# Performance work log

Hardware: AMD Instinct MI355X
Metric: run time of the kernel (lower is better)

## Reference

```python
import jax, jax.numpy as jnp
import numpy as np

E = 8          # num_experts
R = 16         # lora rank
TOP_K = 2
SCALING = 32.0 / 16.0   # lora_alpha / r
D_IN = 4096
D_OUT = 4096


def setup_inputs() -> dict:
    key = jax.random.key(0)
    ks = jax.random.split(key, 6)
    x = jax.random.normal(ks[0], (4, 2048, D_IN), jnp.float32)
    Wb = jax.random.normal(ks[1], (D_OUT, D_IN), jnp.float32) * 0.02
    bias = jax.random.normal(ks[2], (D_OUT,), jnp.float32) * 0.02
    Wr = jax.random.normal(ks[3], (E, D_IN), jnp.float32) * 0.01  # router (normal init, std=0.01)
    A = jax.random.normal(ks[4], (E, R, D_IN), jnp.float32) * (1.0 / np.sqrt(D_IN))  # kaiming-ish
    Bm = jax.random.normal(ks[5], (E, D_OUT, R), jnp.float32) * 0.01  # nonzero for nontrivial baseline
    return {"x": x, "Wb": Wb, "bias": bias, "Wr": Wr, "A": A, "Bm": Bm}


def reference(x, Wb, bias, Wr, A, Bm):
    # x: [B, S, D_IN]
    xf = x.reshape(-1, x.shape[-1])                       # [T, D_IN]
    T = xf.shape[0]

    # Router: softmax -> top-k -> renormalize selected probs
    logits = xf @ Wr.T                                    # [T, E]
    probs = jax.nn.softmax(logits, axis=-1)
    topk_p, topk_i = jax.lax.top_k(probs, TOP_K)          # [T, K]
    topk_p = topk_p / jnp.sum(topk_p, axis=-1, keepdims=True)

    # Dense per-token expert weights via scatter-add (equivalent to masked dispatch/combine)
    w = jnp.zeros((T, E), xf.dtype).at[jnp.arange(T)[:, None], topk_i].add(topk_p)  # [T, E]

    # LoRA: x @ A_e^T @ B_e^T, weighted combine (dropout = identity, p=0)
    h = jnp.einsum('ti,eri->ter', xf, A)                  # [T, E, R] (small: rank-16)
    lora = jnp.einsum('ter,te,eor->to', h, w, Bm) * SCALING  # [T, D_OUT]

    base = xf @ Wb.T + bias                               # [T, D_OUT]
    out = (base + lora).reshape(*x.shape[:-1], D_OUT)
    return out
```

## Files before the change

kernel.cpp:

```cpp
#include <hip/hip_runtime.h>
#include <cmath>

typedef unsigned short ushort_t;
typedef __attribute__((ext_vector_type(8))) short short8;
typedef __attribute__((ext_vector_type(4))) float f32x4;

#define D_IN   4096
#define D_OUT  4096
#define T_TOK  8192
#define E_EXP  8
#define R_RANK 16
#define KCAT   4224
#define SCALE_LORA 2.0f

__device__ __forceinline__ ushort_t f2bf(float f) {
    unsigned int u = __float_as_uint(f);
    u += 0x7fffu + ((u >> 16) & 1u);
    return (ushort_t)(u >> 16);
}

__global__ __launch_bounds__(256) void build_weights(
    const float* __restrict__ Wb, const float* __restrict__ Bm,
    const float* __restrict__ A, ushort_t* __restrict__ Wcat,
    ushort_t* __restrict__ Abf) {
    int b = blockIdx.x;
    int tid = threadIdx.x;
    if (b < D_OUT) {
        const float4* src = (const float4*)(Wb + (size_t)b * D_IN);
        ushort_t* drow = Wcat + (size_t)b * KCAT;
        for (int c4 = tid; c4 < D_IN / 4; c4 += 256) {
            float4 v = src[c4];
            ushort4 o;
            o.x = f2bf(v.x); o.y = f2bf(v.y); o.z = f2bf(v.z); o.w = f2bf(v.w);
            ((ushort4*)drow)[c4] = o;
        }
        if (tid < E_EXP * R_RANK) {
            int e = tid >> 4, r = tid & 15;
            drow[D_IN + tid] = f2bf(Bm[((size_t)e * D_OUT + b) * R_RANK + r]);
        }
    } else {
        int er = b - D_OUT;
        const float4* src = (const float4*)(A + (size_t)er * D_IN);
        ushort_t* drow = Abf + (size_t)er * D_IN;
        for (int c4 = tid; c4 < D_IN / 4; c4 += 256) {
            float4 v = src[c4];
            ushort4 o;
            o.x = f2bf(v.x); o.y = f2bf(v.y); o.z = f2bf(v.z); o.w = f2bf(v.w);
            ((ushort4*)drow)[c4] = o;
        }
    }
}

__global__ __launch_bounds__(256) void router_convert(
    const float* __restrict__ x, const float* __restrict__ Wr,
    ushort_t* __restrict__ xcat, int2* __restrict__ eids,
    float2* __restrict__ wts) {
    __shared__ float sWr[E_EXP * D_IN];
    int tid = threadIdx.x;
    int lane = tid & 63;
    int wave = tid >> 6;
    int tbase = blockIdx.x * 16 + wave * 4;

    {
        const float4* wsrc = (const float4*)Wr;
        float4* wdst = (float4*)sWr;
#pragma unroll
        for (int q = 0; q < 32; q++)
            wdst[tid + q * 256] = wsrc[tid + q * 256];
    }
    __syncthreads();

    float acc[4][E_EXP];
#pragma unroll
    for (int tk = 0; tk < 4; tk++)
#pragma unroll
        for (int e = 0; e < E_EXP; e++) acc[tk][e] = 0.f;

    for (int c4 = lane; c4 < D_IN / 4; c4 += 64) {
        float4 wv[E_EXP];
#pragma unroll
        for (int e = 0; e < E_EXP; e++)
            wv[e] = ((const float4*)(sWr + (size_t)e * D_IN))[c4];
#pragma unroll
        for (int tk = 0; tk < 4; tk++) {
            int t = tbase + tk;
            float4 v = ((const float4*)(x + (size_t)t * D_IN))[c4];
            ushort4 o;
            o.x = f2bf(v.x); o.y = f2bf(v.y); o.z = f2bf(v.z); o.w = f2bf(v.w);
            ((ushort4*)(xcat + (size_t)t * KCAT))[c4] = o;
#pragma unroll
            for (int e = 0; e < E_EXP; e++)
                acc[tk][e] +=
                    v.x * wv[e].x + v.y * wv[e].y + v.z * wv[e].z + v.w * wv[e].w;
        }
    }

#pragma unroll
    for (int tk = 0; tk < 4; tk++)
#pragma unroll
        for (int e = 0; e < E_EXP; e++) {
#pragma unroll
            for (int off = 32; off > 0; off >>= 1)
                acc[tk][e] += __shfl_xor(acc[tk][e], off, 64);
        }
    if (lane == 0) {
#pragma unroll
        for (int tk = 0; tk < 4; tk++) {
            int t = tbase + tk;
            int e0 = 0; float l0 = acc[tk][0];
#pragma unroll
            for (int e = 1; e < E_EXP; e++)
                if (acc[tk][e] > l0) { l0 = acc[tk][e]; e0 = e; }
            int e1 = -1; float l1 = -3.4e38f;
#pragma unroll
            for (int e = 0; e < E_EXP; e++)
                if (e != e0 && acc[tk][e] > l1) { l1 = acc[tk][e]; e1 = e; }
            float w0 = 1.f / (1.f + expf(l1 - l0));
            eids[t] = make_int2(e0, e1);
            wts[t] = make_float2(w0, 1.f - w0);
        }
    }
}

__global__ __launch_bounds__(256) void h_gemm_v(
    const ushort_t* __restrict__ Abf, const int2* __restrict__ eids,
    const float2* __restrict__ wts, ushort_t* __restrict__ xcat) {
    __shared__ __align__(16) ushort_t lA[3][32 * 64];
    __shared__ __align__(16) ushort_t lB[3][128 * 64];
    int tid = threadIdx.x;
    int lane = tid & 63, wave = tid >> 6;
    int rowBase = blockIdx.x * 32;
    const ushort_t* gA = xcat + (size_t)rowBase * KCAT;

    const int srow = tid >> 3;
    const int scol = (((tid & 7) ^ (srow & 7)) << 3);

#define HSTAGE(BUF, KT)                                                        \
    {                                                                          \
        __builtin_amdgcn_global_load_lds(                                      \
            (const __attribute__((address_space(1))) unsigned int*)(           \
                gA + (size_t)srow * KCAT + (KT) + scol),                       \
            (__attribute__((address_space(3))) unsigned int*)(                 \
                &lA[BUF][0] + wave * 512), 16, 0, 0);                          \
        _Pragma("unroll")                                                      \
        for (int q = 0; q < 4; q++) {                                          \
            __builtin_amdgcn_global_load_lds(                                  \
                (const __attribute__((address_space(1))) unsigned int*)(       \
                    Abf + (size_t)(srow + 32 * q) * D_IN + (KT) + scol),       \
                (__attribute__((address_space(3))) unsigned int*)(             \
                    &lB[BUF][0] + q * 2048 + wave * 512), 16, 0, 0);           \
        }                                                                      \
    }

    f32x4 acc[2][2];
#pragma unroll
    for (int i = 0; i < 2; i++)
#pragma unroll
        for (int j = 0; j < 2; j++)
            acc[i][j] = (f32x4){0.f, 0.f, 0.f, 0.f};

    int n0 = wave * 32;
    int row16 = lane & 15;
    int cSwz[2];
#pragma unroll
    for (int kc = 0; kc < 2; kc++)
        cSwz[kc] = (kc * 64 + (lane >> 4) * 16) ^ ((row16 & 7) << 4);

    HSTAGE(0, 0)
    HSTAGE(1, 64)
    asm volatile("s_waitcnt vmcnt(5)" ::: "memory");
    __builtin_amdgcn_s_barrier();

    for (int t = 0; t < 64; ++t) {
        int cur = t % 3;
        int tn = (t + 2 < 64) ? (t + 2) : 63;
        HSTAGE((t + 2) % 3, tn * 64)
        asm volatile("s_waitcnt vmcnt(10)" ::: "memory");
        __builtin_amdgcn_s_barrier();

        short8 af[2][2], bfr[2][2];
#pragma unroll
        for (int i = 0; i < 2; i++)
#pragma unroll
            for (int kc = 0; kc < 2; kc++)
                af[i][kc] = *(const short8*)((const char*)&lA[cur][0] +
                    (i * 16 + row16) * 128 + cSwz[kc]);
#pragma unroll
        for (int j = 0; j < 2; j++)
#pragma unroll
            for (int kc = 0; kc < 2; kc++)
                bfr[j][kc] = *(const short8*)((const char*)&lB[cur][0] +
                    (n0 + j * 16 + row16) * 128 + cSwz[kc]);

        __builtin_amdgcn_s_setprio(1);
#pragma unroll
        for (int i = 0; i < 2; i++)
#pragma unroll
            for (int j = 0; j < 2; j++) {
                acc[i][j] = __builtin_amdgcn_mfma_f32_16x16x32_bf16(
                    af[i][0], bfr[j][0], acc[i][j], 0, 0, 0);
                acc[i][j] = __builtin_amdgcn_mfma_f32_16x16x32_bf16(
                    af[i][1], bfr[j][1], acc[i][j], 0, 0, 0);
            }
        __builtin_amdgcn_s_setprio(0);
        __builtin_amdgcn_s_barrier();
    }

#pragma unroll
    for (int i = 0; i < 2; i++) {
        int rbase = rowBase + i * 16 + (lane >> 4) * 4;
#pragma unroll
        for (int reg = 0; reg < 4; reg++) {
            int t = rbase + reg;
            int2 e = eids[t];
            float2 w = wts[t];
#pragma unroll
            for (int j = 0; j < 2; j++) {
                int c = n0 + j * 16 + (lane & 15);
                int ce = c >> 4;
                float coef = (ce == e.x) ? (SCALE_LORA * w.x)
                           : ((ce == e.y) ? (SCALE_LORA * w.y) : 0.f);
                xcat[(size_t)t * KCAT + D_IN + c] = f2bf(coef * acc[i][j][reg]);
            }
        }
    }
#undef HSTAGE
}

#define NKT 66
#define NIT 33

__global__ __launch_bounds__(512, 2) void gemm_bt_main(
    const ushort_t* __restrict__ Am, const ushort_t* __restrict__ Bmat,
    float* __restrict__ C, const float* __restrict__ bias) {
    __shared__ __align__(16) ushort_t lds[2][2][2][128][64];
    const int lda = KCAT, ldb = KCAT, ldc = D_OUT;
    int tid = threadIdx.x;
    int lane = tid & 63, wave = tid >> 6;
    int wm = wave >> 2, wn = wave & 3;

    int id = ((blockIdx.x & 7) << 6) | (blockIdx.x >> 3);
    int band = id >> 6, wi = id & 63;
    int mt = ((band >> 1) << 3) | (wi & 7);
    int nt = ((band & 1) << 3) | (wi >> 3);
    const int rowBase = mt * 256, colBase = nt * 256;

    const ushort_t* gA = Am + (size_t)rowBase * lda;
    const ushort_t* gB = Bmat + (size_t)colBase * ldb;

    const int srow = tid >> 3;
    const int scol = (((tid & 7) ^ (srow & 7)) << 3);

#define STAGE(MAT, SRC, LD, BUF, KT)                                           \
    {                                                                          \
        _Pragma("unroll")                                                      \
        for (int h = 0; h < 2; h++) {                                          \
            _Pragma("unroll")                                                  \
            for (int q = 0; q < 2; q++) {                                      \
                __builtin_amdgcn_global_load_lds(                              \
                    (const __attribute__((address_space(1))) unsigned int*)(   \
                        (SRC) + (size_t)(h * 128 + q * 64 + srow) * (LD) +     \
                        (KT) + scol),                                          \
                    (__attribute__((address_space(3))) unsigned int*)(         \
                        &lds[BUF][MAT][h][0][0] + q * 4096 + wave * 512),      \
                    16, 0, 0);                                                 \
            }                                                                  \
        }                                                                      \
    }

    int cSwz[2];
#pragma unroll
    for (int kc = 0; kc < 2; kc++)
        cSwz[kc] = (kc * 64 + (lane >> 4) * 16) ^ ((lane & 7) << 4);
    const int rOff = (lane & 15) * 128;
    const int bRow = (wn & 1) * 64 * 128;

    const char* baseA = (const char*)&lds[0][0][wm][0][0];
    const char* baseB = (const char*)&lds[0][1][wn >> 1][0][0];

    f32x4 acc[8][4];
#pragma unroll
    for (int i = 0; i < 8; i++)
#pragma unroll
        for (int j = 0; j < 4; j++) acc[i][j] = (f32x4){0.f, 0.f, 0.f, 0.f};

    short8 aF[4][2], bF[2][2];

#define READ_A(BUF, S)                                                         \
    _Pragma("unroll")                                                          \
    for (int m4 = 0; m4 < 4; m4++) {                                           \
        _Pragma("unroll")                                                      \
        for (int kc = 0; kc < 2; kc++)                                         \
            aF[m4][kc] = *(const short8*)(baseA + (BUF) * 65536 +              \
                ((S) * 4 + m4) * 2048 + rOff + cSwz[kc]);                      \
    }

#define READ_B(BUF, U)                                                         \
    _Pragma("unroll")                                                          \
    for (int n2 = 0; n2 < 2; n2++) {                                           \
        _Pragma("unroll")                                                      \
        for (int kc = 0; kc < 2; kc++)                                         \
            bF[n2][kc] = *(const short8*)(baseB + (BUF) * 65536 + bRow +       \
                ((U) * 2 + n2) * 2048 + rOff + cSwz[kc]);                      \
    }

#define MFMA16(S, U)                                                           \
    __builtin_amdgcn_s_setprio(1);                                             \
    _Pragma("unroll")                                                          \
    for (int m4 = 0; m4 < 4; m4++) {                                           \
        _Pragma("unroll")                                                      \
        for (int n2 = 0; n2 < 2; n2++) {                                       \
            _Pragma("unroll")                                                  \
            for (int kc = 0; kc < 2; kc++)                                     \
                acc[(S) * 4 + m4][(U) * 2 + n2] =                              \
                    __builtin_amdgcn_mfma_f32_16x16x32_bf16(                   \
                        aF[m4][kc], bF[n2][kc],                                \
                        acc[(S) * 4 + m4][(U) * 2 + n2], 0, 0, 0);             \
        }                                                                      \
    }                                                                          \
    __builtin_amdgcn_s_setprio(0);

#define MIDBAR()                                                               \
    __builtin_amdgcn_s_barrier();                                              \
    asm volatile("s_waitcnt lgkmcnt(0)" ::: "memory");

#define ENDBAR() __builtin_amdgcn_s_barrier();

    STAGE(0, gA, lda, 0, 0)
    STAGE(1, gB, ldb, 0, 0)
    STAGE(0, gA, lda, 1, 64)
    asm volatile("s_waitcnt vmcnt(4)" ::: "memory");
    __builtin_amdgcn_s_barrier();

    for (int it = 0; it < NIT; ++it) {
        int ktB1 = (2 * it + 1) * 64;
        int t2 = 2 * it + 2; if (t2 > NKT - 1) t2 = NKT - 1;
        int t3 = 2 * it + 3; if (t3 > NKT - 1) t3 = NKT - 1;
        int kt2 = t2 * 64, kt3 = t3 * 64;

        READ_A(0, 0) READ_B(0, 0)
        STAGE(1, gB, ldb, 1, ktB1)
        MIDBAR() MFMA16(0, 0) ENDBAR()

        READ_B(0, 1)
        MIDBAR() MFMA16(0, 1) ENDBAR()

        READ_A(0, 1)
        MIDBAR() MFMA16(1, 1) ENDBAR()

        READ_B(0, 0)
        STAGE(0, gA, lda, 0, kt2)
        MIDBAR() MFMA16(1, 0)
        asm volatile("s_waitcnt vmcnt(4)" ::: "memory");
        ENDBAR()

        READ_A(1, 0) READ_B(1, 0)
        STAGE(1, gB, ldb, 0, kt2)
        MIDBAR() MFMA16(0, 0) ENDBAR()

        READ_B(1, 1)
        MIDBAR() MFMA16(0, 1) ENDBAR()

        READ_A(1, 1)
        MIDBAR() MFMA16(1, 1) ENDBAR()

        READ_B(1, 0)
        STAGE(0, gA, lda, 1, kt3)
        MIDBAR() MFMA16(1, 0)
        asm volatile("s_waitcnt vmcnt(4)" ::: "memory");
        ENDBAR()
    }

    int r0 = rowBase + wm * 128 + (lane >> 4) * 4;
    int c0 = colBase + wn * 64 + (lane & 15);
#pragma unroll
    for (int mf = 0; mf < 8; mf++) {
#pragma unroll
        for (int nf = 0; nf < 4; nf++) {
            int cc = c0 + nf * 16;
            float badd = bias[cc];
#pragma unroll
            for (int reg = 0; reg < 4; reg++)
                C[(size_t)(r0 + mf * 16 + reg) * ldc + cc] = acc[mf][nf][reg] + badd;
        }
    }
}

extern "C" void kernel_launch(void* const* d_in, const int* in_sizes, int n_in,
                              void* d_out, int out_size, void* d_ws, size_t ws_size,
                              hipStream_t stream) {
    const float* x    = (const float*)d_in[0];
    const float* Wb   = (const float*)d_in[1];
    const float* bias = (const float*)d_in[2];
    const float* Wr   = (const float*)d_in[3];
    const float* A    = (const float*)d_in[4];
    const float* Bm   = (const float*)d_in[5];
    float* out = (float*)d_out;

    char* p = (char*)d_ws;
    ushort_t* xcat = (ushort_t*)p; p += (size_t)T_TOK * KCAT * 2;
    ushort_t* Wcat = (ushort_t*)p; p += (size_t)D_OUT * KCAT * 2;
    ushort_t* Abf  = (ushort_t*)p; p += (size_t)(E_EXP * R_RANK) * D_IN * 2;
    int2*     eids = (int2*)p;     p += (size_t)T_TOK * sizeof(int2);
    float2*   wts  = (float2*)p;   p += (size_t)T_TOK * sizeof(float2);

    build_weights<<<D_OUT + E_EXP * R_RANK, 256, 0, stream>>>(Wb, Bm, A, Wcat, Abf);
    router_convert<<<T_TOK / 16, 256, 0, stream>>>(x, Wr, xcat, eids, wts);
    h_gemm_v<<<T_TOK / 32, 256, 0, stream>>>(Abf, eids, wts, xcat);
    gemm_bt_main<<<(T_TOK / 256) * (D_OUT / 256), 512, 0, stream>>>(xcat, Wcat, out, bias);
}
```

Measured before the change: 559.8 us.

## Switch main GEMM to 32x32x16 MFMA and drop LDS staging in router

The main bf16 GEMM moves from 16x16x32 MFMA tiles to 32x32x16 tiles. This halves the instruction count and reduces LDS fragment reads per FLOP, and the fragment read schedule and epilogue store mapping are reworked to fit. Separately, the router kernel no longer copies the 128KB router weight matrix into shared memory. It reads it directly from global/L2 and processes 2 tokens per wave with twice as many blocks, which raises occupancy but re-reads Wr from cache more often.

```diff
diff --git a/kernel.cpp b/kernel.cpp
--- a/kernel.cpp
+++ b/kernel.cpp
@@ -4,6 +4,7 @@
 typedef unsigned short ushort_t;
 typedef __attribute__((ext_vector_type(8))) short short8;
 typedef __attribute__((ext_vector_type(4))) float f32x4;
+typedef __attribute__((ext_vector_type(16))) float f32x16;
 
 #define D_IN   4096
 #define D_OUT  4096
@@ -55,24 +56,14 @@
     const float* __restrict__ x, const float* __restrict__ Wr,
     ushort_t* __restrict__ xcat, int2* __restrict__ eids,
     float2* __restrict__ wts) {
-    __shared__ float sWr[E_EXP * D_IN];
     int tid = threadIdx.x;
     int lane = tid & 63;
     int wave = tid >> 6;
-    int tbase = blockIdx.x * 16 + wave * 4;
-
-    {
-        const float4* wsrc = (const float4*)Wr;
-        float4* wdst = (float4*)sWr;
-#pragma unroll
-        for (int q = 0; q < 32; q++)
-            wdst[tid + q * 256] = wsrc[tid + q * 256];
-    }
-    __syncthreads();
-
-    float acc[4][E_EXP];
-#pragma unroll
-    for (int tk = 0; tk < 4; tk++)
+    int tbase = blockIdx.x * 8 + wave * 2;
+
+    float acc[2][E_EXP];
+#pragma unroll
+    for (int tk = 0; tk < 2; tk++)
 #pragma unroll
         for (int e = 0; e < E_EXP; e++) acc[tk][e] = 0.f;
 
@@ -80,9 +71,9 @@
         float4 wv[E_EXP];
 #pragma unroll
         for (int e = 0; e < E_EXP; e++)
-            wv[e] = ((const float4*)(sWr + (size_t)e * D_IN))[c4];
-#pragma unroll
-        for (int tk = 0; tk < 4; tk++) {
+            wv[e] = ((const float4*)(Wr + (size_t)e * D_IN))[c4];
+#pragma unroll
+        for (int tk = 0; tk < 2; tk++) {
             int t = tbase + tk;
             float4 v = ((const float4*)(x + (size_t)t * D_IN))[c4];
             ushort4 o;
@@ -96,7 +87,7 @@
     }
 
 #pragma unroll
-    for (int tk = 0; tk < 4; tk++)
+    for (int tk = 0; tk < 2; tk++)
 #pragma unroll
         for (int e = 0; e < E_EXP; e++) {
 #pragma unroll
@@ -105,7 +96,7 @@
         }
     if (lane == 0) {
 #pragma unroll
-        for (int tk = 0; tk < 4; tk++) {
+        for (int tk = 0; tk < 2; tk++) {
             int t = tbase + tk;
             int e0 = 0; float l0 = acc[tk][0];
 #pragma unroll
@@ -268,54 +259,56 @@
         }                                                                      \
     }
 
-    int cSwz[2];
-#pragma unroll
-    for (int kc = 0; kc < 2; kc++)
-        cSwz[kc] = (kc * 64 + (lane >> 4) * 16) ^ ((lane & 7) << 4);
-    const int rOff = (lane & 15) * 128;
+    int kOff[4];
+#pragma unroll
+    for (int ks = 0; ks < 4; ks++)
+        kOff[ks] = (ks * 32 + ((lane >> 5) << 4)) ^ ((lane & 7) << 4);
+    const int rOff = (lane & 31) * 128;
     const int bRow = (wn & 1) * 64 * 128;
 
     const char* baseA = (const char*)&lds[0][0][wm][0][0];
-    const char* baseB = (const char*)&lds[0][1][wn >> 1][0][0];
-
-    f32x4 acc[8][4];
-#pragma unroll
-    for (int i = 0; i < 8; i++)
-#pragma unroll
-        for (int j = 0; j < 4; j++) acc[i][j] = (f32x4){0.f, 0.f, 0.f, 0.f};
-
-    short8 aF[4][2], bF[2][2];
-
-#define READ_A(BUF, S)                                                         \
+    const char* baseB = (const char*)&lds[0][1][wn >> 1][0][0] + bRow;
+
+    f32x16 acc[4][2];
+#pragma unroll
+    for (int i = 0; i < 4; i++)
+#pragma unroll
+        for (int j = 0; j < 2; j++)
+#pragma unroll
+            for (int r = 0; r < 16; r++) acc[i][j][r] = 0.f;
+
+    short8 A1[2][2], A2[2][2], bF[2][2];
+
+#define READ_AX(REG, BUF, MP, KP)                                              \
     _Pragma("unroll")                                                          \
-    for (int m4 = 0; m4 < 4; m4++) {                                           \
+    for (int m2 = 0; m2 < 2; m2++) {                                           \
         _Pragma("unroll")                                                      \
-        for (int kc = 0; kc < 2; kc++)                                         \
-            aF[m4][kc] = *(const short8*)(baseA + (BUF) * 65536 +              \
-                ((S) * 4 + m4) * 2048 + rOff + cSwz[kc]);                      \
-    }
-
-#define READ_B(BUF, U)                                                         \
+        for (int k2 = 0; k2 < 2; k2++)                                         \
+            REG[m2][k2] = *(const short8*)(baseA + (BUF) * 65536 +             \
+                ((MP) * 2 + m2) * 4096 + rOff + kOff[(KP) * 2 + k2]);          \
+    }
+
+#define READ_B32(BUF, KP)                                                      \
     _Pragma("unroll")                                                          \
     for (int n2 = 0; n2 < 2; n2++) {                                           \
         _Pragma("unroll")                                                      \
-        for (int kc = 0; kc < 2; kc++)                                         \
-            bF[n2][kc] = *(const short8*)(baseB + (BUF) * 65536 + bRow +       \
-                ((U) * 2 + n2) * 2048 + rOff + cSwz[kc]);                      \
-    }
-
-#define MFMA16(S, U)                                                           \
+        for (int k2 = 0; k2 < 2; k2++)                                         \
+            bF[n2][k2] = *(const short8*)(baseB + (BUF) * 65536 +              \
+                n2 * 4096 + rOff + kOff[(KP) * 2 + k2]);                       \
+    }
+
+#define MFMA8(REG, MP)                                                         \
     __builtin_amdgcn_s_setprio(1);                                             \
     _Pragma("unroll")                                                          \
-    for (int m4 = 0; m4 < 4; m4++) {                                           \
+    for (int k2 = 0; k2 < 2; k2++) {                                           \
         _Pragma("unroll")                                                      \
-        for (int n2 = 0; n2 < 2; n2++) {                                       \
+        for (int m2 = 0; m2 < 2; m2++) {                                       \
             _Pragma("unroll")                                                  \
-            for (int kc = 0; kc < 2; kc++)                                     \
-                acc[(S) * 4 + m4][(U) * 2 + n2] =                              \
-                    __builtin_amdgcn_mfma_f32_16x16x32_bf16(                   \
-                        aF[m4][kc], bF[n2][kc],                                \
-                        acc[(S) * 4 + m4][(U) * 2 + n2], 0, 0, 0);             \
+            for (int n2 = 0; n2 < 2; n2++)                                     \
+                acc[(MP) * 2 + m2][n2] =                                       \
+                    __builtin_amdgcn_mfma_f32_32x32x16_bf16(                   \
+                        REG[m2][k2], bF[n2][k2],                               \
+                        acc[(MP) * 2 + m2][n2], 0, 0, 0);                      \
         }                                                                      \
     }                                                                          \
     __builtin_amdgcn_s_setprio(0);
@@ -338,50 +331,50 @@
         int t3 = 2 * it + 3; if (t3 > NKT - 1) t3 = NKT - 1;
         int kt2 = t2 * 64, kt3 = t3 * 64;
 
-        READ_A(0, 0) READ_B(0, 0)
+        READ_AX(A1, 0, 0, 0) READ_B32(0, 0)
         STAGE(1, gB, ldb, 1, ktB1)
-        MIDBAR() MFMA16(0, 0) ENDBAR()
-
-        READ_B(0, 1)
-        MIDBAR() MFMA16(0, 1) ENDBAR()
-
-        READ_A(0, 1)
-        MIDBAR() MFMA16(1, 1) ENDBAR()
-
-        READ_B(0, 0)
+        MIDBAR() MFMA8(A1, 0) ENDBAR()
+
+        READ_AX(A2, 0, 1, 0)
+        MIDBAR() MFMA8(A2, 1) ENDBAR()
+
+        READ_AX(A1, 0, 0, 1) READ_AX(A2, 0, 1, 1) READ_B32(0, 1)
+        MIDBAR() MFMA8(A1, 0) ENDBAR()
+
         STAGE(0, gA, lda, 0, kt2)
-        MIDBAR() MFMA16(1, 0)
+        MIDBAR() MFMA8(A2, 1)
         asm volatile("s_waitcnt vmcnt(4)" ::: "memory");
         ENDBAR()
 
-        READ_A(1, 0) READ_B(1, 0)
+        READ_AX(A1, 1, 0, 0) READ_B32(1, 0)
         STAGE(1, gB, ldb, 0, kt2)
-        MIDBAR() MFMA16(0, 0) ENDBAR()
-
-        READ_B(1, 1)
-        MIDBAR() MFMA16(0, 1) ENDBAR()
-
-        READ_A(1, 1)
-        MIDBAR() MFMA16(1, 1) ENDBAR()
-
-        READ_B(1, 0)
+        MIDBAR() MFMA8(A1, 0) ENDBAR()
+
+        READ_AX(A2, 1, 1, 0)
+        MIDBAR() MFMA8(A2, 1) ENDBAR()
+
+        READ_AX(A1, 1, 0, 1) READ_AX(A2, 1, 1, 1) READ_B32(1, 1)
+        MIDBAR() MFMA8(A1, 0) ENDBAR()
+
         STAGE(0, gA, lda, 1, kt3)
-        MIDBAR() MFMA16(1, 0)
+        MIDBAR() MFMA8(A2, 1)
         asm volatile("s_waitcnt vmcnt(4)" ::: "memory");
         ENDBAR()
     }
 
-    int r0 = rowBase + wm * 128 + (lane >> 4) * 4;
-    int c0 = colBase + wn * 64 + (lane & 15);
-#pragma unroll
-    for (int mf = 0; mf < 8; mf++) {
-#pragma unroll
-        for (int nf = 0; nf < 4; nf++) {
-            int cc = c0 + nf * 16;
+    int r0 = rowBase + wm * 128 + ((lane >> 5) << 2);
+    int c0 = colBase + wn * 64 + (lane & 31);
+#pragma unroll
+    for (int mtl = 0; mtl < 4; mtl++) {
+#pragma unroll
+        for (int ntl = 0; ntl < 2; ntl++) {
+            int cc = c0 + ntl * 32;
             float badd = bias[cc];
 #pragma unroll
-            for (int reg = 0; reg < 4; reg++)
-                C[(size_t)(r0 + mf * 16 + reg) * ldc + cc] = acc[mf][nf][reg] + badd;
+            for (int reg = 0; reg < 16; reg++) {
+                int rr = r0 + mtl * 32 + (reg & 3) + ((reg >> 2) << 3);
+                C[(size_t)rr * ldc + cc] = acc[mtl][ntl][reg] + badd;
+            }
         }
     }
 }
@@ -405,7 +398,7 @@
     float2*   wts  = (float2*)p;   p += (size_t)T_TOK * sizeof(float2);
 
     build_weights<<<D_OUT + E_EXP * R_RANK, 256, 0, stream>>>(Wb, Bm, A, Wcat, Abf);
-    router_convert<<<T_TOK / 16, 256, 0, stream>>>(x, Wr, xcat, eids, wts);
+    router_convert<<<T_TOK / 8, 256, 0, stream>>>(x, Wr, xcat, eids, wts);
     h_gemm_v<<<T_TOK / 32, 256, 0, stream>>>(Abf, eids, wts, xcat);
     gemm_bt_main<<<(T_TOK / 256) * (D_OUT / 256), 512, 0, stream>>>(xcat, Wcat, out, bias);
 }
```

Result: slower. 590.0 us (+5.4%).
